# Optimization experiments

Hardware: AMD Instinct MI355X
Metric: run time of the kernel (lower is better)

Reference implementation:

```python
import jax, jax.numpy as jnp
import numpy as np
import math

B = 2048
INPUT_SIZE = 1024
OUTPUT_SIZE = 512
SPONGE = 1024
ACT = 256
REC = 256
STORE = ACT + REC  # 512
DEPTH = 8
BDEPTH = 10
NEUTRAL_C = 1.0
SQRT2 = math.sqrt(2.0)


def _make_structure():
    # Deterministic stand-in for the module's random.sample-based recall wiring.
    rng = np.random.RandomState(0)
    half = (SPONGE + 1) // 2
    shuffle_perm = np.array([i // 2 + (i % 2) * half for i in range(SPONGE)], dtype=np.int64)
    unused = []
    recall = []
    for i in range(DEPTH):
        unused.extend(range(i * STORE, (i + 1) * STORE))
        sel = rng.choice(len(unused), size=REC, replace=False)
        sel_set = set(sel.tolist())
        recall.append([unused[k] for k in sorted(sel_set)])
        unused = [u for k, u in enumerate(unused) if k not in sel_set]
    out_mem = np.array(sorted(unused), dtype=np.int64)  # 2048 leftover memory columns
    bf_size = len(out_mem) + SPONGE  # 3072
    bf_depth = int(math.ceil(math.log2(bf_size)))  # 12
    bf_half = (bf_size + 1) // 2
    bf_perm = np.array([i // 2 + (i % 2) * bf_half for i in range(bf_size)], dtype=np.int64)
    return shuffle_perm, np.array(recall, dtype=np.int64), out_mem, bf_perm, bf_size, bf_depth


def setup_inputs() -> dict:
    key = jax.random.key(0)
    ks = jax.random.split(key, 6)
    shuffle_perm, recall_idx, out_mem_idx, bf_perm, bf_size, bf_depth = _make_structure()
    return {
        "X": jax.random.normal(ks[0], (B, INPUT_SIZE), jnp.float32),
        "scales": jnp.ones((INPUT_SIZE,), jnp.float32),
        "angles": jax.random.uniform(ks[1], (DEPTH, BDEPTH, SPONGE // 2), jnp.float32) * (2 * math.pi),
        "act_bias": jax.random.normal(ks[2], (DEPTH, ACT), jnp.float32),
        "act_activation": jax.random.normal(ks[3], (DEPTH, ACT), jnp.float32),
        "act_curvature": jax.random.normal(ks[4], (DEPTH, ACT), jnp.float32),
        "bf_angles": jax.random.uniform(ks[5], (bf_depth, bf_size // 2), jnp.float32) * (2 * math.pi),
        "shuffle_perm": jnp.asarray(shuffle_perm),
        "recall_idx": jnp.asarray(recall_idx),
        "output_mem_idx": jnp.asarray(out_mem_idx),
        "bf_perm": jnp.asarray(bf_perm),
    }


def _base_activation(x, c):
    # In the source, `a` is overwritten with torch.tensor(1.0), so a == 1.
    t = (math.pi / 4) / c
    y0 = (1.0 / c) * (1.0 / SQRT2 - math.cos(math.pi / 2))  # = 1/(c*sqrt(2))
    m0 = math.sin(math.pi / 2)  # = 1
    y1 = (1.0 / c) * (1.0 / SQRT2 - 1.0)
    m1 = math.sin(0.0)  # = 0
    mid = (1.0 / c) * (1.0 / SQRT2 - jnp.cos(math.pi / 4 + c * x))
    return jnp.where(x > t, y0 + m0 * (x - t), jnp.where(x < -t, y1 + m1 * (x + t), mid))


def _butterfly(x, angles, perm):
    # angles: [n_layers, exch]; shuffle -> Givens rotation per pair, extra passthrough
    exch = angles.shape[1]
    for j in range(angles.shape[0]):
        s = x[:, perm]
        x1, x2 = s[:, :exch], s[:, exch:2 * exch]
        ca, sa = jnp.cos(angles[j]), jnp.sin(angles[j])
        x = jnp.concatenate([ca * x1 + sa * x2, -sa * x1 + ca * x2, s[:, 2 * exch:]], axis=1)
    return x


def reference(X, scales, angles, act_bias, act_activation, act_curvature, bf_angles,
              shuffle_perm, recall_idx, output_mem_idx, bf_perm):
    Xs = X * scales
    sponge = Xs[:, :SPONGE]  # input_size == sponge_size: no zero pad, memory[0] is empty
    mem = jnp.zeros((Xs.shape[0], DEPTH * STORE), Xs.dtype)
    for i in range(DEPTH):
        sponge = _butterfly(sponge, angles[i], shuffle_perm)
        x1 = sponge[:, STORE:STORE + ACT] + act_bias[i]  # activation_position == store_size
        c = 0.5 * NEUTRAL_C * (act_curvature[i] + jnp.sqrt(act_curvature[i] ** 2 + 1.0))
        ap = _base_activation(x1, c)
        am = _base_activation(-x1, c)
        act_out = jnp.stack([ap, am], axis=2).reshape(ap.shape[0], 2 * ACT)  # interleave +/-
        mem = mem.at[:, i * STORE:(i + 1) * STORE].set(sponge[:, :STORE])
        recall = mem[:, recall_idx[i]]  # indices only address already-filled columns
        # [act_out | sponge[store:act_pos] (empty) | sponge[act_pos+ACT:] | recall]
        sponge = jnp.concatenate([act_out, sponge[:, STORE + ACT:], recall], axis=1)
    pre = jnp.concatenate([mem[:, output_mem_idx], sponge], axis=1)  # [B, 3072]
    out = _butterfly(pre, bf_angles, bf_perm)
    return out[:, :OUTPUT_SIZE]
```

## Files before the change

kernel.cpp:

```cpp
#include <hip/hip_runtime.h>
#include <math.h>

#define NB 2048
#define DEPTH 8

#define FTAB_OFF    0
#define BF01_OFF    81920
#define BFF_OFF     88064
#define ACT4_OFF    98304
#define PHYSA_OFF   106496
#define PHYSR_OFF   110592
#define PHYSO2_OFF  112640

__global__ void setup_kernel(const float* __restrict__ angles,
                             const float* __restrict__ bf_angles,
                             const float* __restrict__ act_bias,
                             const float* __restrict__ act_curv,
                             const int* __restrict__ recall_idx,
                             const int* __restrict__ out_mem_idx,
                             float* __restrict__ ws) {
    __shared__ int physL[4096];
    if (blockIdx.x < 200) {
        int id = blockIdx.x * 256 + threadIdx.x;
        if (id < 40960) {
            int w = id & 3, t = (id >> 2) & 255, dg = id >> 10;
            int d = dg / 5, g = dg - 5 * d;
            int a = 2 * (t & 127) + (t >> 7);
            int pair = (w == 0) ? a : (w == 1) ? (a + 256)
                     : (w == 2) ? (2 * a) : (2 * a + 1);
            int st = 2 * g + (w >> 1);
            float ang = angles[(d * 10 + st) * 512 + pair];
            float s, c; sincosf(ang, &s, &c);
            ws[FTAB_OFF + 2 * id]     = c;
            ws[FTAB_OFF + 2 * id + 1] = s;
        } else if (id < 44032) {
            int e = id - 40960;
            int w = e & 3; int ti = e >> 2;
            int t = ti / 3; int i = ti - 3 * t;
            int a = t + 256 * i;
            int pair = (w == 0) ? a : (w == 1) ? (a + 768)
                     : (w == 2) ? (2 * a) : (2 * a + 1);
            int stage = (w < 2) ? 0 : 1;
            float ang = bf_angles[stage * 1536 + pair];
            float s, c; sincosf(ang, &s, &c);
            ws[BF01_OFF + 2 * e]     = c;
            ws[BF01_OFF + 2 * e + 1] = s;
        } else if (id < 49152) {
            int e = id - 44032;
            int f = e >> 10; int rem = e & 1023; int t = rem >> 2; int w = rem & 3;
            int P;
            if (f == 0) P = 3 * t;
            else if (f < 4) { int k = 8 - 2 * f;
                              P = ((t >> (2 * f)) * (768 >> k)) + (t & ((256 >> k) - 1)); }
            else P = t;
            int pair = (w == 0) ? P : (w == 1) ? (P + 768)
                     : (w == 2) ? (2 * P) : (2 * P + 1);
            int stage = (w < 2) ? (2 + 2 * f) : (3 + 2 * f);
            float ang = bf_angles[stage * 1536 + pair];
            float s, c; sincosf(ang, &s, &c);
            ws[BFF_OFF + 2 * e]     = c;
            ws[BFF_OFF + 2 * e + 1] = s;
        } else if (id < 51200) {
            int ida = id - 49152;
            float cu = act_curv[ida];
            float c  = 0.5f * (cu + sqrtf(cu * cu + 1.0f));
            ((float4*)(ws + ACT4_OFF))[ida] =
                make_float4(act_bias[ida], c, 1.0f / c, 0.0f);
        }
    } else {
        int tid = threadIdx.x;
        for (int e = tid; e < 4096; e += 256) {
            int v = e, p;
            for (;;) {
                int d = v >> 9, j = v & 511;
                if (d == 0)  { p = j; break; }
                if (j < 256) { p = 256 + d * 256 + j; break; }
                v = recall_idx[(d - 1) * 256 + (j - 256)];
            }
            physL[e] = p;
        }
        __syncthreads();
        int* pa = (int*)(ws + PHYSA_OFF);
        for (int e = tid; e < 2048; e += 256) {
            int d = e >> 8, t = e & 255;
            int a = 2 * (t & 127) + (t >> 7);
            pa[2 * e]     = physL[d * 512 + 2 * a];
            pa[2 * e + 1] = physL[d * 512 + 2 * a + 1];
        }
        int* pr = (int*)(ws + PHYSR_OFF);
        for (int e = tid; e < 2048; e += 256)
            pr[e] = physL[recall_idx[e]];
        int* po = (int*)(ws + PHYSO2_OFF);
        for (int e = tid; e < 3072; e += 256) {
            int tt = e / 12; int r = e - 12 * tt; int i = r >> 2; int k = r & 3;
            int a = tt + 256 * i;
            int tl2 = a >> 1, th2 = a & 1;
            int pos = tl2 + 1536 * th2 + 384 * k;
            po[e] = (pos < 2048) ? physL[out_mem_idx[pos]] : 2304 + (pos - 2048);
        }
    }
}

__device__ __forceinline__ float actf(float x, float c, float ic) {
    const float is2 = 0.70710678118654752f;
    float tt = 0.78539816339744831f * ic;
    float y0 = is2 * ic;
    float y1 = (is2 - 1.0f) * ic;
    float mid = ic * (is2 - __cosf(0.78539816339744831f + c * x));
    return x > tt ? (y0 + (x - tt)) : (x < -tt ? y1 : mid);
}

__launch_bounds__(256, 4)
__global__ void sponge_kernel(const float* __restrict__ X,
                              const float* __restrict__ scales,
                              const float* __restrict__ ws,
                              float* __restrict__ out) {
    __shared__ float lds[8704];
    float* L0 = lds;
    float* L1 = lds + 4352;
    const int t = threadIdx.x;
    const int rowA = blockIdx.x * 2;

    const float4* bf01  = (const float4*)(ws + BF01_OFF);
    const float4* bff   = (const float4*)(ws + BFF_OFF);
    const float4* act4  = (const float4*)(ws + ACT4_OFF);
    const int2* physA  = (const int2*)(ws + PHYSA_OFF);
    const int*  physr  = (const int*)(ws + PHYSR_OFF);
    const int*  physo2 = (const int*)(ws + PHYSO2_OFF);

    const int tl = t & 127, th = t >> 7;
    const int b  = tl + th * 512;
    const int Wb = 2 * (tl & 15) + 32 * th + 64 * (tl >> 4);
    const int Rb = (tl & 1) + 2 * ((tl >> 2) & 15) + 32 * ((tl >> 1) & 1)
                 + 64 * (tl >> 6) + 512 * th;
    const int u  = t - 128;

    float hA0, hA1, hA2, hA3, hB0, hB1, hB2, hB3;
    {
        const float* Xr0 = X + (size_t)rowA * 1024;
        const float* Xr1 = Xr0 + 1024;
        float s0 = scales[b],       s1 = scales[b + 128];
        float s2 = scales[b + 256], s3 = scales[b + 384];
        hA0 = Xr0[b] * s0; hA1 = Xr0[b + 128] * s1;
        hA2 = Xr0[b + 256] * s2; hA3 = Xr0[b + 384] * s3;
        hB0 = Xr1[b] * s0; hB1 = Xr1[b + 128] * s1;
        hB2 = Xr1[b + 256] * s2; hB3 = Xr1[b + 384] * s3;
    }

    int woff = 2304, roff = 3328;
    const float4* ft = (const float4*)(ws + FTAB_OFF) + 2 * t;

#define DQUAD(cA, cB, i0, i1, i2, i3, F0, F1, F2, F3)                    \
    { float g0 =  (cA).x * (i0) + (cA).y * (i2);                         \
      float g2 = -(cA).y * (i0) + (cA).x * (i2);                         \
      float g1 =  (cA).z * (i1) + (cA).w * (i3);                         \
      float g3 = -(cA).w * (i1) + (cA).z * (i3);                         \
      F0 =  (cB).x * g0 + (cB).y * g1;                                   \
      F2 = -(cB).y * g0 + (cB).x * g1;                                   \
      F1 =  (cB).z * g2 + (cB).w * g3;                                   \
      F3 = -(cB).w * g2 + (cB).z * g3; }

    for (int d = 0; d < DEPTH; ++d) {
        for (int g = 0; g < 5; ++g) {
            float4 csA = ft[0], csB = ft[1]; ft += 512;
            float fA0, fA1, fA2, fA3, fB0, fB1, fB2, fB3;
            DQUAD(csA, csB, hA0, hA1, hA2, hA3, fA0, fA1, fA2, fA3);
            DQUAD(csA, csB, hB0, hB1, hB2, hB3, fB0, fB1, fB2, fB3);
            if (g < 4) {
                *(float2*)(L0 + woff + Wb)       = make_float2(fA0, fA1);
                *(float2*)(L0 + woff + Wb + 512) = make_float2(fA2, fA3);
                *(float2*)(L1 + woff + Wb)       = make_float2(fB0, fB1);
                *(float2*)(L1 + woff + Wb + 512) = make_float2(fB2, fB3);
                { int tmp = woff; woff = roff; roff = tmp; }
                __syncthreads();
                const float* e0 = L0 + roff + Rb;
                const float* e1 = L1 + roff + Rb;
                hA0 = e0[0]; hA1 = e0[128]; hA2 = e0[256]; hA3 = e0[384];
                hB0 = e1[0]; hB1 = e1[128]; hB2 = e1[256]; hB3 = e1[384];
            } else {
                int2 pm = physA[d * 256 + t];
                L0[pm.x] = fA0; L0[pm.y] = fA1;
                L1[pm.x] = fB0; L1[pm.y] = fB1;
                *(float2*)(L0 + woff + 4 * tl + 2 * th) = make_float2(fA2, fA3);
                *(float2*)(L1 + woff + 4 * tl + 2 * th) = make_float2(fB2, fB3);
                { int tmp = woff; woff = roff; roff = tmp; }
                int r0 = 0, r1 = 0;
                float4 a0, a1, a2, a3;
                if (t < 128) {
                    int k0 = t >> 1;
                    a0 = act4[d * 256 + k0];
                    a1 = act4[d * 256 + k0 + 64];
                    a2 = act4[d * 256 + k0 + 128];
                    a3 = act4[d * 256 + k0 + 192];
                } else {
                    r0 = physr[d * 256 + u];
                    r1 = physr[d * 256 + u + 128];
                }
                __syncthreads();
                const float* Z0 = L0 + roff;
                const float* Z1 = L1 + roff;
                if (t < 128) {
                    int k0 = t >> 1;
                    float sgn = (t & 1) ? -1.0f : 1.0f;
                    hA0 = actf(sgn * (Z0[k0]       + a0.x), a0.y, a0.z);
                    hA1 = actf(sgn * (Z0[k0 + 64]  + a1.x), a1.y, a1.z);
                    hA2 = actf(sgn * (Z0[k0 + 128] + a2.x), a2.y, a2.z);
                    hA3 = actf(sgn * (Z0[k0 + 192] + a3.x), a3.y, a3.z);
                    hB0 = actf(sgn * (Z1[k0]       + a0.x), a0.y, a0.z);
                    hB1 = actf(sgn * (Z1[k0 + 64]  + a1.x), a1.y, a1.z);
                    hB2 = actf(sgn * (Z1[k0 + 128] + a2.x), a2.y, a2.z);
                    hB3 = actf(sgn * (Z1[k0 + 192] + a3.x), a3.y, a3.z);
                } else {
                    hA0 = Z0[256 + u]; hA1 = Z0[384 + u];
                    hB0 = Z1[256 + u]; hB1 = Z1[384 + u];
                    hA2 = L0[r0]; hA3 = L0[r1];
                    hB2 = L1[r0]; hB3 = L1[r1];
                }
            }
        }
    }

    L0[2304 + b] = hA0; L0[2304 + b + 128] = hA1;
    L0[2304 + b + 256] = hA2; L0[2304 + b + 384] = hA3;
    L1[2304 + b] = hB0; L1[2304 + b + 128] = hB1;
    L1[2304 + b + 256] = hB2; L1[2304 + b + 384] = hB3;
    __syncthreads();

    float vA0, vA1, vA2, vA3, vA4, vA5, vA6, vA7, vA8, vA9, vA10, vA11;
    float vB0, vB1, vB2, vB3, vB4, vB5, vB6, vB7, vB8, vB9, vB10, vB11;
    {
        int4 pg = ((const int4*)(physo2 + t * 12))[0];
        vA0 = L0[pg.x]; vA1 = L0[pg.y]; vA2 = L0[pg.z]; vA3 = L0[pg.w];
        vB0 = L1[pg.x]; vB1 = L1[pg.y]; vB2 = L1[pg.z]; vB3 = L1[pg.w];
        pg = ((const int4*)(physo2 + t * 12))[1];
        vA4 = L0[pg.x]; vA5 = L0[pg.y]; vA6 = L0[pg.z]; vA7 = L0[pg.w];
        vB4 = L1[pg.x]; vB5 = L1[pg.y]; vB6 = L1[pg.z]; vB7 = L1[pg.w];
        pg = ((const int4*)(physo2 + t * 12))[2];
        vA8 = L0[pg.x]; vA9 = L0[pg.y]; vA10 = L0[pg.z]; vA11 = L0[pg.w];
        vB8 = L1[pg.x]; vB9 = L1[pg.y]; vB10 = L1[pg.z]; vB11 = L1[pg.w];
    }
    __syncthreads();

#define BF01_STEP(i, qA0, qA1, qA2, qA3, qB0, qB1, qB2, qB3)                        \
    {                                                                               \
        float4 c01 = bf01[(t * 3 + (i)) * 2];                                       \
        float4 c23 = bf01[(t * 3 + (i)) * 2 + 1];                                   \
        float y0, y1, y2, y3;                                                       \
        DQUAD(c01, c23, qA0, qA1, qA2, qA3, y0, y1, y2, y3);                        \
        *(float2*)(L0 + 2 * t + 512 * (i))        = make_float2(y0, y1);            \
        *(float2*)(L0 + 2 * t + 512 * (i) + 1536) = make_float2(y2, y3);            \
        DQUAD(c01, c23, qB0, qB1, qB2, qB3, y0, y1, y2, y3);                        \
        *(float2*)(L1 + 2 * t + 512 * (i))        = make_float2(y0, y1);            \
        *(float2*)(L1 + 2 * t + 512 * (i) + 1536) = make_float2(y2, y3);            \
    }
    BF01_STEP(0, vA0, vA1, vA2, vA3, vB0, vB1, vB2, vB3)
    BF01_STEP(1, vA4, vA5, vA6, vA7, vB4, vB5, vB6, vB7)
    BF01_STEP(2, vA8, vA9, vA10, vA11, vB8, vB9, vB10, vB11)
#undef BF01_STEP
    __syncthreads();

#pragma unroll
    for (int f = 0; f < 4; ++f) {
        int P;
        if (f == 0) P = 3 * t;
        else { const int k = 8 - 2 * f;
               P = ((t >> (2 * f)) * (768 >> k)) + (t & ((256 >> k) - 1)); }
        int base = (P >> 1) + (P & 1) * 1536;
        float4 csS = bff[(f * 256 + t) * 2];
        float4 csT = bff[(f * 256 + t) * 2 + 1];
        float xA1p = L0[base], xA1q = L0[base + 384];
        float xA2p = L0[base + 768], xA2q = L0[base + 1152];
        float xB1p = L1[base], xB1q = L1[base + 384];
        float xB2p = L1[base + 768], xB2q = L1[base + 1152];
        float o1P =  csS.x * xA1p + csS.y * xA2p;
        float o2P = -csS.y * xA1p + csS.x * xA2p;
        float o1Q =  csS.z * xA1q + csS.w * xA2q;
        float o2Q = -csS.w * xA1q + csS.z * xA2q;
        float yA0 =  csT.x * o1P + csT.y * o1Q;
        float yA2 = -csT.y * o1P + csT.x * o1Q;
        float yA1 =  csT.z * o2P + csT.w * o2Q;
        float yA3 = -csT.w * o2P + csT.z * o2Q;
        o1P =  csS.x * xB1p + csS.y * xB2p;
        o2P = -csS.y * xB1p + csS.x * xB2p;
        o1Q =  csS.z * xB1q + csS.w * xB2q;
        o2Q = -csS.w * xB1q + csS.z * xB2q;
        float yB0 =  csT.x * o1P + csT.y * o1Q;
        float yB2 = -csT.y * o1P + csT.x * o1Q;
        float yB1 =  csT.z * o2P + csT.w * o2Q;
        float yB3 = -csT.w * o2P + csT.z * o2Q;
        __syncthreads();
        *(float2*)(L0 + 2 * P)        = make_float2(yA0, yA1);
        *(float2*)(L0 + 2 * P + 1536) = make_float2(yA2, yA3);
        *(float2*)(L1 + 2 * P)        = make_float2(yB0, yB1);
        *(float2*)(L1 + 2 * P + 1536) = make_float2(yB2, yB3);
        __syncthreads();
    }

    {
        int base = (t >> 1) + (t & 1) * 1536;
        float4 csS = bff[(4 * 256 + t) * 2];
        float4 csT = bff[(4 * 256 + t) * 2 + 1];
        float x1p = L0[base], x1q = L0[base + 384];
        float x2p = L0[base + 768], x2q = L0[base + 1152];
        float o1P =  csS.x * x1p + csS.y * x2p;
        float o2P = -csS.y * x1p + csS.x * x2p;
        float o1Q =  csS.z * x1q + csS.w * x2q;
        float o2Q = -csS.w * x1q + csS.z * x2q;
        *(float2*)(out + (size_t)rowA * 512 + 2 * t) =
            make_float2(csT.x * o1P + csT.y * o1Q, csT.z * o2P + csT.w * o2Q);
        x1p = L1[base]; x1q = L1[base + 384];
        x2p = L1[base + 768]; x2q = L1[base + 1152];
        o1P =  csS.x * x1p + csS.y * x2p;
        o2P = -csS.y * x1p + csS.x * x2p;
        o1Q =  csS.z * x1q + csS.w * x2q;
        o2Q = -csS.w * x1q + csS.z * x2q;
        *(float2*)(out + (size_t)(rowA + 1) * 512 + 2 * t) =
            make_float2(csT.x * o1P + csT.y * o1Q, csT.z * o2P + csT.w * o2Q);
    }
#undef DQUAD
}

extern "C" void kernel_launch(void* const* d_in, const int* in_sizes, int n_in,
                              void* d_out, int out_size, void* d_ws, size_t ws_size,
                              hipStream_t stream) {
    const float* X          = (const float*)d_in[0];
    const float* scales     = (const float*)d_in[1];
    const float* angles     = (const float*)d_in[2];
    const float* act_bias   = (const float*)d_in[3];
    const float* act_curv   = (const float*)d_in[5];
    const float* bf_angles  = (const float*)d_in[6];
    const int*   recall_idx  = (const int*)d_in[8];
    const int*   out_mem_idx = (const int*)d_in[9];

    float* ws = (float*)d_ws;

    setup_kernel<<<201, 256, 0, stream>>>(angles, bf_angles, act_bias, act_curv,
                                          recall_idx, out_mem_idx, ws);
    sponge_kernel<<<NB / 2, 256, 0, stream>>>(X, scales, ws, (float*)d_out);
}
```

Baseline: 119.4 us.

## Interleave the two batch rows in shared memory to vectorize LDS accesses

Shared memory now holds the two rows each block processes interleaved (row A and row B side by side) instead of in two separate buffers. Every scalar LDS read and write becomes a float2 or float4 access, and the precomputed index tables are doubled to match. This roughly halves the number of LDS instructions, though wider accesses can raise bank conflicts on the scattered gathers. The setup kernel also switches sincosf to the fast __sincosf intrinsic, which is less accurate for large angles.

```diff
diff --git a/kernel.cpp b/kernel.cpp
--- a/kernel.cpp
+++ b/kernel.cpp
@@ -11,6 +11,9 @@
 #define PHYSA_OFF   106496
 #define PHYSR_OFF   110592
 #define PHYSO2_OFF  112640
+
+#define MB0 4608
+#define MB1 6656
 
 __global__ void setup_kernel(const float* __restrict__ angles,
                              const float* __restrict__ bf_angles,
@@ -30,7 +33,7 @@
                      : (w == 2) ? (2 * a) : (2 * a + 1);
             int st = 2 * g + (w >> 1);
             float ang = angles[(d * 10 + st) * 512 + pair];
-            float s, c; sincosf(ang, &s, &c);
+            float s, c; __sincosf(ang, &s, &c);
             ws[FTAB_OFF + 2 * id]     = c;
             ws[FTAB_OFF + 2 * id + 1] = s;
         } else if (id < 44032) {
@@ -42,7 +45,7 @@
                      : (w == 2) ? (2 * a) : (2 * a + 1);
             int stage = (w < 2) ? 0 : 1;
             float ang = bf_angles[stage * 1536 + pair];
-            float s, c; sincosf(ang, &s, &c);
+            float s, c; __sincosf(ang, &s, &c);
             ws[BF01_OFF + 2 * e]     = c;
             ws[BF01_OFF + 2 * e + 1] = s;
         } else if (id < 49152) {
@@ -57,7 +60,7 @@
                      : (w == 2) ? (2 * P) : (2 * P + 1);
             int stage = (w < 2) ? (2 + 2 * f) : (3 + 2 * f);
             float ang = bf_angles[stage * 1536 + pair];
-            float s, c; sincosf(ang, &s, &c);
+            float s, c; __sincosf(ang, &s, &c);
             ws[BFF_OFF + 2 * e]     = c;
             ws[BFF_OFF + 2 * e + 1] = s;
         } else if (id < 51200) {
@@ -84,19 +87,20 @@
         for (int e = tid; e < 2048; e += 256) {
             int d = e >> 8, t = e & 255;
             int a = 2 * (t & 127) + (t >> 7);
-            pa[2 * e]     = physL[d * 512 + 2 * a];
-            pa[2 * e + 1] = physL[d * 512 + 2 * a + 1];
+            pa[2 * e]     = 2 * physL[d * 512 + 2 * a];
+            pa[2 * e + 1] = 2 * physL[d * 512 + 2 * a + 1];
         }
         int* pr = (int*)(ws + PHYSR_OFF);
         for (int e = tid; e < 2048; e += 256)
-            pr[e] = physL[recall_idx[e]];
+            pr[e] = 2 * physL[recall_idx[e]];
         int* po = (int*)(ws + PHYSO2_OFF);
         for (int e = tid; e < 3072; e += 256) {
             int tt = e / 12; int r = e - 12 * tt; int i = r >> 2; int k = r & 3;
             int a = tt + 256 * i;
             int tl2 = a >> 1, th2 = a & 1;
             int pos = tl2 + 1536 * th2 + 384 * k;
-            po[e] = (pos < 2048) ? physL[out_mem_idx[pos]] : 2304 + (pos - 2048);
+            po[e] = (pos < 2048) ? 2 * physL[out_mem_idx[pos]]
+                                 : MB0 + 2 * (pos - 2048);
         }
     }
 }
@@ -115,9 +119,7 @@
                               const float* __restrict__ scales,
                               const float* __restrict__ ws,
                               float* __restrict__ out) {
-    __shared__ float lds[8704];
-    float* L0 = lds;
-    float* L1 = lds + 4352;
+    __shared__ float L[8704];
     const int t = threadIdx.x;
     const int rowA = blockIdx.x * 2;
 
@@ -130,9 +132,12 @@
 
     const int tl = t & 127, th = t >> 7;
     const int b  = tl + th * 512;
+    const int a  = 2 * tl + th;
     const int Wb = 2 * (tl & 15) + 32 * th + 64 * (tl >> 4);
     const int Rb = (tl & 1) + 2 * ((tl >> 2) & 15) + 32 * ((tl >> 1) & 1)
                  + 64 * (tl >> 6) + 512 * th;
+    const int WI = 2 * Wb;
+    const int RI = 2 * Rb;
     const int u  = t - 128;
 
     float hA0, hA1, hA2, hA3, hB0, hB1, hB2, hB3;
@@ -147,7 +152,7 @@
         hB2 = Xr1[b + 256] * s2; hB3 = Xr1[b + 384] * s3;
     }
 
-    int woff = 2304, roff = 3328;
+    int woff = MB0, roff = MB1;
     const float4* ft = (const float4*)(ws + FTAB_OFF) + 2 * t;
 
 #define DQUAD(cA, cB, i0, i1, i2, i3, F0, F1, F2, F3)                    \
@@ -167,22 +172,21 @@
             DQUAD(csA, csB, hA0, hA1, hA2, hA3, fA0, fA1, fA2, fA3);
             DQUAD(csA, csB, hB0, hB1, hB2, hB3, fB0, fB1, fB2, fB3);
             if (g < 4) {
-                *(float2*)(L0 + woff + Wb)       = make_float2(fA0, fA1);
-                *(float2*)(L0 + woff + Wb + 512) = make_float2(fA2, fA3);
-                *(float2*)(L1 + woff + Wb)       = make_float2(fB0, fB1);
-                *(float2*)(L1 + woff + Wb + 512) = make_float2(fB2, fB3);
+                *(float4*)(L + woff + WI)        = make_float4(fA0, fB0, fA1, fB1);
+                *(float4*)(L + woff + WI + 1024) = make_float4(fA2, fB2, fA3, fB3);
                 { int tmp = woff; woff = roff; roff = tmp; }
                 __syncthreads();
-                const float* e0 = L0 + roff + Rb;
-                const float* e1 = L1 + roff + Rb;
-                hA0 = e0[0]; hA1 = e0[128]; hA2 = e0[256]; hA3 = e0[384];
-                hB0 = e1[0]; hB1 = e1[128]; hB2 = e1[256]; hB3 = e1[384];
+                float2 e0 = *(const float2*)(L + roff + RI);
+                float2 e1 = *(const float2*)(L + roff + RI + 256);
+                float2 e2 = *(const float2*)(L + roff + RI + 512);
+                float2 e3 = *(const float2*)(L + roff + RI + 768);
+                hA0 = e0.x; hB0 = e0.y; hA1 = e1.x; hB1 = e1.y;
+                hA2 = e2.x; hB2 = e2.y; hA3 = e3.x; hB3 = e3.y;
             } else {
                 int2 pm = physA[d * 256 + t];
-                L0[pm.x] = fA0; L0[pm.y] = fA1;
-                L1[pm.x] = fB0; L1[pm.y] = fB1;
-                *(float2*)(L0 + woff + 4 * tl + 2 * th) = make_float2(fA2, fA3);
-                *(float2*)(L1 + woff + 4 * tl + 2 * th) = make_float2(fB2, fB3);
+                *(float2*)(L + pm.x) = make_float2(fA0, fB0);
+                *(float2*)(L + pm.y) = make_float2(fA1, fB1);
+                *(float4*)(L + woff + 4 * a) = make_float4(fA2, fB2, fA3, fB3);
                 { int tmp = woff; woff = roff; roff = tmp; }
                 int r0 = 0, r1 = 0;
                 float4 a0, a1, a2, a3;
@@ -197,65 +201,69 @@
                     r1 = physr[d * 256 + u + 128];
                 }
                 __syncthreads();
-                const float* Z0 = L0 + roff;
-                const float* Z1 = L1 + roff;
+                const float* Z = L + roff;
                 if (t < 128) {
                     int k0 = t >> 1;
                     float sgn = (t & 1) ? -1.0f : 1.0f;
-                    hA0 = actf(sgn * (Z0[k0]       + a0.x), a0.y, a0.z);
-                    hA1 = actf(sgn * (Z0[k0 + 64]  + a1.x), a1.y, a1.z);
-                    hA2 = actf(sgn * (Z0[k0 + 128] + a2.x), a2.y, a2.z);
-                    hA3 = actf(sgn * (Z0[k0 + 192] + a3.x), a3.y, a3.z);
-                    hB0 = actf(sgn * (Z1[k0]       + a0.x), a0.y, a0.z);
-                    hB1 = actf(sgn * (Z1[k0 + 64]  + a1.x), a1.y, a1.z);
-                    hB2 = actf(sgn * (Z1[k0 + 128] + a2.x), a2.y, a2.z);
-                    hB3 = actf(sgn * (Z1[k0 + 192] + a3.x), a3.y, a3.z);
+                    float2 z0 = *(const float2*)(Z + 2 * k0);
+                    float2 z1 = *(const float2*)(Z + 2 * k0 + 128);
+                    float2 z2 = *(const float2*)(Z + 2 * k0 + 256);
+                    float2 z3 = *(const float2*)(Z + 2 * k0 + 384);
+                    hA0 = actf(sgn * (z0.x + a0.x), a0.y, a0.z);
+                    hB0 = actf(sgn * (z0.y + a0.x), a0.y, a0.z);
+                    hA1 = actf(sgn * (z1.x + a1.x), a1.y, a1.z);
+                    hB1 = actf(sgn * (z1.y + a1.x), a1.y, a1.z);
+                    hA2 = actf(sgn * (z2.x + a2.x), a2.y, a2.z);
+                    hB2 = actf(sgn * (z2.y + a2.x), a2.y, a2.z);
+                    hA3 = actf(sgn * (z3.x + a3.x), a3.y, a3.z);
+                    hB3 = actf(sgn * (z3.y + a3.x), a3.y, a3.z);
                 } else {
-                    hA0 = Z0[256 + u]; hA1 = Z0[384 + u];
-                    hB0 = Z1[256 + u]; hB1 = Z1[384 + u];
-                    hA2 = L0[r0]; hA3 = L0[r1];
-                    hB2 = L1[r0]; hB3 = L1[r1];
+                    float2 k0v = *(const float2*)(Z + 512 + 2 * u);
+                    float2 k1v = *(const float2*)(Z + 768 + 2 * u);
+                    float2 rc0 = *(const float2*)(L + r0);
+                    float2 rc1 = *(const float2*)(L + r1);
+                    hA0 = k0v.x; hB0 = k0v.y;
+                    hA1 = k1v.x; hB1 = k1v.y;
+                    hA2 = rc0.x; hB2 = rc0.y;
+                    hA3 = rc1.x; hB3 = rc1.y;
                 }
             }
         }
     }
 
-    L0[2304 + b] = hA0; L0[2304 + b + 128] = hA1;
-    L0[2304 + b + 256] = hA2; L0[2304 + b + 384] = hA3;
-    L1[2304 + b] = hB0; L1[2304 + b + 128] = hB1;
-    L1[2304 + b + 256] = hB2; L1[2304 + b + 384] = hB3;
+    *(float2*)(L + MB0 + 2 * b)       = make_float2(hA0, hB0);
+    *(float2*)(L + MB0 + 2 * b + 256) = make_float2(hA1, hB1);
+    *(float2*)(L + MB0 + 2 * b + 512) = make_float2(hA2, hB2);
+    *(float2*)(L + MB0 + 2 * b + 768) = make_float2(hA3, hB3);
     __syncthreads();
 
-    float vA0, vA1, vA2, vA3, vA4, vA5, vA6, vA7, vA8, vA9, vA10, vA11;
-    float vB0, vB1, vB2, vB3, vB4, vB5, vB6, vB7, vB8, vB9, vB10, vB11;
+    float2 w0, w1, w2, w3, w4, w5, w6, w7, w8, w9, w10, w11;
     {
         int4 pg = ((const int4*)(physo2 + t * 12))[0];
-        vA0 = L0[pg.x]; vA1 = L0[pg.y]; vA2 = L0[pg.z]; vA3 = L0[pg.w];
-        vB0 = L1[pg.x]; vB1 = L1[pg.y]; vB2 = L1[pg.z]; vB3 = L1[pg.w];
+        w0 = *(const float2*)(L + pg.x); w1 = *(const float2*)(L + pg.y);
+        w2 = *(const float2*)(L + pg.z); w3 = *(const float2*)(L + pg.w);
         pg = ((const int4*)(physo2 + t * 12))[1];
-        vA4 = L0[pg.x]; vA5 = L0[pg.y]; vA6 = L0[pg.z]; vA7 = L0[pg.w];
-        vB4 = L1[pg.x]; vB5 = L1[pg.y]; vB6 = L1[pg.z]; vB7 = L1[pg.w];
+        w4 = *(const float2*)(L + pg.x); w5 = *(const float2*)(L + pg.y);
+        w6 = *(const float2*)(L + pg.z); w7 = *(const float2*)(L + pg.w);
         pg = ((const int4*)(physo2 + t * 12))[2];
-        vA8 = L0[pg.x]; vA9 = L0[pg.y]; vA10 = L0[pg.z]; vA11 = L0[pg.w];
-        vB8 = L1[pg.x]; vB9 = L1[pg.y]; vB10 = L1[pg.z]; vB11 = L1[pg.w];
+        w8 = *(const float2*)(L + pg.x); w9 = *(const float2*)(L + pg.y);
+        w10 = *(const float2*)(L + pg.z); w11 = *(const float2*)(L + pg.w);
     }
     __syncthreads();
 
-#define BF01_STEP(i, qA0, qA1, qA2, qA3, qB0, qB1, qB2, qB3)                        \
+#define BF01_STEP(i, q0, q1, q2, q3)                                                \
     {                                                                               \
         float4 c01 = bf01[(t * 3 + (i)) * 2];                                       \
         float4 c23 = bf01[(t * 3 + (i)) * 2 + 1];                                   \
-        float y0, y1, y2, y3;                                                       \
-        DQUAD(c01, c23, qA0, qA1, qA2, qA3, y0, y1, y2, y3);                        \
-        *(float2*)(L0 + 2 * t + 512 * (i))        = make_float2(y0, y1);            \
-        *(float2*)(L0 + 2 * t + 512 * (i) + 1536) = make_float2(y2, y3);            \
-        DQUAD(c01, c23, qB0, qB1, qB2, qB3, y0, y1, y2, y3);                        \
-        *(float2*)(L1 + 2 * t + 512 * (i))        = make_float2(y0, y1);            \
-        *(float2*)(L1 + 2 * t + 512 * (i) + 1536) = make_float2(y2, y3);            \
-    }
-    BF01_STEP(0, vA0, vA1, vA2, vA3, vB0, vB1, vB2, vB3)
-    BF01_STEP(1, vA4, vA5, vA6, vA7, vB4, vB5, vB6, vB7)
-    BF01_STEP(2, vA8, vA9, vA10, vA11, vB8, vB9, vB10, vB11)
+        float yA0, yA1, yA2, yA3, yB0, yB1, yB2, yB3;                               \
+        DQUAD(c01, c23, q0.x, q1.x, q2.x, q3.x, yA0, yA1, yA2, yA3);                \
+        DQUAD(c01, c23, q0.y, q1.y, q2.y, q3.y, yB0, yB1, yB2, yB3);                \
+        *(float4*)(L + 4 * t + 1024 * (i))        = make_float4(yA0, yB0, yA1, yB1);\
+        *(float4*)(L + 4 * t + 1024 * (i) + 3072) = make_float4(yA2, yB2, yA3, yB3);\
+    }
+    BF01_STEP(0, w0, w1, w2, w3)
+    BF01_STEP(1, w4, w5, w6, w7)
+    BF01_STEP(2, w8, w9, w10, w11)
 #undef BF01_STEP
     __syncthreads();
 
@@ -265,55 +273,53 @@
         if (f == 0) P = 3 * t;
         else { const int k = 8 - 2 * f;
                P = ((t >> (2 * f)) * (768 >> k)) + (t & ((256 >> k) - 1)); }
-        int base = (P >> 1) + (P & 1) * 1536;
+        int base = 2 * ((P >> 1) + (P & 1) * 1536);
         float4 csS = bff[(f * 256 + t) * 2];
         float4 csT = bff[(f * 256 + t) * 2 + 1];
-        float xA1p = L0[base], xA1q = L0[base + 384];
-        float xA2p = L0[base + 768], xA2q = L0[base + 1152];
-        float xB1p = L1[base], xB1q = L1[base + 384];
-        float xB2p = L1[base + 768], xB2q = L1[base + 1152];
-        float o1P =  csS.x * xA1p + csS.y * xA2p;
-        float o2P = -csS.y * xA1p + csS.x * xA2p;
-        float o1Q =  csS.z * xA1q + csS.w * xA2q;
-        float o2Q = -csS.w * xA1q + csS.z * xA2q;
+        float2 x1p = *(const float2*)(L + base);
+        float2 x1q = *(const float2*)(L + base + 768);
+        float2 x2p = *(const float2*)(L + base + 1536);
+        float2 x2q = *(const float2*)(L + base + 2304);
+        float o1P =  csS.x * x1p.x + csS.y * x2p.x;
+        float o2P = -csS.y * x1p.x + csS.x * x2p.x;
+        float o1Q =  csS.z * x1q.x + csS.w * x2q.x;
+        float o2Q = -csS.w * x1q.x + csS.z * x2q.x;
         float yA0 =  csT.x * o1P + csT.y * o1Q;
         float yA2 = -csT.y * o1P + csT.x * o1Q;
         float yA1 =  csT.z * o2P + csT.w * o2Q;
         float yA3 = -csT.w * o2P + csT.z * o2Q;
-        o1P =  csS.x * xB1p + csS.y * xB2p;
-        o2P = -csS.y * xB1p + csS.x * xB2p;
-        o1Q =  csS.z * xB1q + csS.w * xB2q;
-        o2Q = -csS.w * xB1q + csS.z * xB2q;
+        o1P =  csS.x * x1p.y + csS.y * x2p.y;
+        o2P = -csS.y * x1p.y + csS.x * x2p.y;
+        o1Q =  csS.z * x1q.y + csS.w * x2q.y;
+        o2Q = -csS.w * x1q.y + csS.z * x2q.y;
         float yB0 =  csT.x * o1P + csT.y * o1Q;
         float yB2 = -csT.y * o1P + csT.x * o1Q;
         float yB1 =  csT.z * o2P + csT.w * o2Q;
         float yB3 = -csT.w * o2P + csT.z * o2Q;
         __syncthreads();
-        *(float2*)(L0 + 2 * P)        = make_float2(yA0, yA1);
-        *(float2*)(L0 + 2 * P + 1536) = make_float2(yA2, yA3);
-        *(float2*)(L1 + 2 * P)        = make_float2(yB0, yB1);
-        *(float2*)(L1 + 2 * P + 1536) = make_float2(yB2, yB3);
+        *(float4*)(L + 4 * P)        = make_float4(yA0, yB0, yA1, yB1);
+        *(float4*)(L + 4 * P + 3072) = make_float4(yA2, yB2, yA3, yB3);
         __syncthreads();
     }
 
     {
-        int base = (t >> 1) + (t & 1) * 1536;
+        int base = 2 * ((t >> 1) + (t & 1) * 1536);
         float4 csS = bff[(4 * 256 + t) * 2];
         float4 csT = bff[(4 * 256 + t) * 2 + 1];
-        float x1p = L0[base], x1q = L0[base + 384];
-        float x2p = L0[base + 768], x2q = L0[base + 1152];
-        float o1P =  csS.x * x1p + csS.y * x2p;
-        float o2P = -csS.y * x1p + csS.x * x2p;
-        float o1Q =  csS.z * x1q + csS.w * x2q;
-        float o2Q = -csS.w * x1q + csS.z * x2q;
+        float2 x1p = *(const float2*)(L + base);
+        float2 x1q = *(const float2*)(L + base + 768);
+        float2 x2p = *(const float2*)(L + base + 1536);
+        float2 x2q = *(const float2*)(L + base + 2304);
+        float o1P =  csS.x * x1p.x + csS.y * x2p.x;
+        float o2P = -csS.y * x1p.x + csS.x * x2p.x;
+        float o1Q =  csS.z * x1q.x + csS.w * x2q.x;
+        float o2Q = -csS.w * x1q.x + csS.z * x2q.x;
         *(float2*)(out + (size_t)rowA * 512 + 2 * t) =
             make_float2(csT.x * o1P + csT.y * o1Q, csT.z * o2P + csT.w * o2Q);
-        x1p = L1[base]; x1q = L1[base + 384];
-        x2p = L1[base + 768]; x2q = L1[base + 1152];
-        o1P =  csS.x * x1p + csS.y * x2p;
-        o2P = -csS.y * x1p + csS.x * x2p;
-        o1Q =  csS.z * x1q + csS.w * x2q;
-        o2Q = -csS.w * x1q + csS.z * x2q;
+        o1P =  csS.x * x1p.y + csS.y * x2p.y;
+        o2P = -csS.y * x1p.y + csS.x * x2p.y;
+        o1Q =  csS.z * x1q.y + csS.w * x2q.y;
+        o2Q = -csS.w * x1q.y + csS.z * x2q.y;
         *(float2*)(out + (size_t)(rowA + 1) * 512 + 2 * t) =
             make_float2(csT.x * o1P + csT.y * o1Q, csT.z * o2P + csT.w * o2Q);
     }
```

New measurement: 118.1 us. No clear change (-1.1%).
